# Performance work log

Measured on AMD Instinct MI355X. Metric: run time of the kernel, lower is better.

The kernel has to match this reference:

```python
import jax, jax.numpy as jnp
import numpy as np

B, T, U, D = 2, 512, 48, 512
H, K = 1024, 128  # hidden_channels, num_classes; fc1 in = 2*D = 1024


def setup_inputs() -> dict:
    key = jax.random.key(0)
    ks = jax.random.split(key, 9)
    s = 0.02
    return {
        "img_feature": jax.random.normal(ks[0], (B, T, D), jnp.float32),
        "label_feature": jax.random.normal(ks[1], (B, U, D), jnp.float32),
        "masks": jnp.ones((B, 1, T), jnp.float32),
        "W1": jax.random.normal(ks[2], (H, 2 * D), jnp.float32) * s,
        "b1": jnp.zeros((H,), jnp.float32),
        "W2": jax.random.normal(ks[3], (K, H), jnp.float32) * s,
        "b2": jnp.zeros((K,), jnp.float32),
        "conv_w": jax.random.normal(ks[4], (K, D), jnp.float32) * s,
        "conv_b": jnp.zeros((K,), jnp.float32),
    }


def reference(img_feature, label_feature, masks, W1, b1, W2, b2, conv_w, conv_b):
    # pointwise Conv1d over img features: (B,T,D) -> (B,K,T), masked
    img_seg_score = (jnp.einsum('btd,kd->bkt', img_feature, conv_w)
                     + conv_b[None, :, None]) * masks
    # fc1(cat(label, img)) == label @ Wl^T + img @ Wi^T + b1 (broadcast add),
    # avoiding the O(B*U*T*2D) repeat+cat intermediate.
    d = label_feature.shape[-1]
    Wl, Wi = W1[:, :d], W1[:, d:]
    lab = jnp.einsum('bud,hd->buh', label_feature, Wl)  # (B,U,H)
    img = jnp.einsum('btd,hd->bth', img_feature, Wi)    # (B,T,H)
    h = jnp.tanh(lab[:, :, None, :] + img[:, None, :, :] + b1)  # (B,U,T,H)
    joint = jnp.einsum('buth,kh->butk', h, W2) + b2
    joint_score = jax.nn.log_softmax(joint, axis=-1)
    return (img_seg_score, joint_score)
```

## Files before the change

### kernel.cpp

```cpp
#include <hip/hip_runtime.h>
#include <math.h>

#define BB 2
#define TT 512
#define UU 48
#define DD 512
#define HH 1024
#define KK 128

typedef __bf16 bf16x8 __attribute__((ext_vector_type(8)));
typedef float floatx4 __attribute__((ext_vector_type(4)));

__device__ __forceinline__ float tanh_fast(float x) {
    float x2 = x * x;
    float num = x * fmaf(x2, x2 + 105.0f, 945.0f);
    float den = fmaf(x2, fmaf(x2, 15.0f, 420.0f), 945.0f);
    float r = num * __fdividef(1.0f, den);
    return fminf(1.0f, fmaxf(-1.0f, r));
}

__global__ __launch_bounds__(256) void mid_kernel2(
    const float* __restrict__ img, const float* __restrict__ labf,
    const float* __restrict__ W1, const float* __restrict__ W2,
    const float* __restrict__ conv_w,
    const float* __restrict__ b1, const float* __restrict__ conv_b,
    const float* __restrict__ masks,
    __bf16* __restrict__ imgHb, __bf16* __restrict__ labHb,
    __bf16* __restrict__ W2s, float* __restrict__ seg_out) {
    int bid = blockIdx.x, tid = threadIdx.x;
    if (bid >= 312) {
        int base = (bid - 312) * 256 + tid;
#pragma unroll
        for (int i = 0; i < 32; ++i) {
            int o = base + i * 4096;
            int hg = o >> 10, kk2 = (o >> 3) & 127, hl = o & 7;
            W2s[o] = (__bf16)W2[(size_t)kk2 * HH + hg * 8 + hl];
        }
        return;
    }
    __shared__ __align__(16) __bf16 a_s[32][72];
    __shared__ __align__(16) __bf16 w_s[8192];
    const float* Arow;
    const float* Wbase;
    int r0, n0b, wstride, region;
    if (bid < 256) {
        region = 0; Arow = img; Wbase = W1 + 512; wstride = 1024;
        r0 = (bid & 31) * 32; n0b = (bid >> 5) * 128;
    } else if (bid < 280) {
        region = 1; Arow = labf; Wbase = W1; wstride = 1024;
        int i = bid - 256; r0 = (i % 3) * 32; n0b = (i / 3) * 128;
    } else {
        region = 2; Arow = img; Wbase = conv_w; wstride = 512;
        r0 = (bid - 280) * 32; n0b = 0;
    }
    int lane = tid & 63, wv = tid >> 6;
    int m0 = (wv & 1) * 16, n0w = (wv >> 1) * 64;
    int q = lane >> 4, r = lane & 15;
    int arow = tid >> 3, acol = (tid & 7) * 8;
    floatx4 acc[4] = {};
    for (int c = 0; c < 8; ++c) {
        int cb = c * 64;
        {
            const float* ap = &Arow[(size_t)(r0 + arow) * DD + cb + acol];
            float4 a0 = *(const float4*)ap;
            float4 a1 = *(const float4*)(ap + 4);
            bf16x8 av;
            av[0] = (__bf16)a0.x; av[1] = (__bf16)a0.y;
            av[2] = (__bf16)a0.z; av[3] = (__bf16)a0.w;
            av[4] = (__bf16)a1.x; av[5] = (__bf16)a1.y;
            av[6] = (__bf16)a1.z; av[7] = (__bf16)a1.w;
            *(bf16x8*)&a_s[arow][acol] = av;
        }
#pragma unroll
        for (int i2 = 0; i2 < 4; ++i2) {
            int g = i2 * 256 + tid;
            int kg = g >> 7, n = g & 127;
            const float* wp = &Wbase[(size_t)(n0b + n) * wstride + cb + kg * 8];
            float4 w0 = *(const float4*)wp;
            float4 w1 = *(const float4*)(wp + 4);
            bf16x8 wvv;
            wvv[0] = (__bf16)w0.x; wvv[1] = (__bf16)w0.y;
            wvv[2] = (__bf16)w0.z; wvv[3] = (__bf16)w0.w;
            wvv[4] = (__bf16)w1.x; wvv[5] = (__bf16)w1.y;
            wvv[6] = (__bf16)w1.z; wvv[7] = (__bf16)w1.w;
            *(bf16x8*)&w_s[g * 8] = wvv;
        }
        __syncthreads();
#pragma unroll
        for (int kt = 0; kt < 2; ++kt) {
            bf16x8 af = *(const bf16x8*)&a_s[m0 + r][kt * 32 + q * 8];
#pragma unroll
            for (int nt = 0; nt < 4; ++nt) {
                bf16x8 bfv = *(const bf16x8*)
                    &w_s[((kt * 4 + q) * 128 + n0w + nt * 16 + r) * 8];
                acc[nt] = __builtin_amdgcn_mfma_f32_16x16x32_bf16(
                    af, bfv, acc[nt], 0, 0, 0);
            }
        }
        __syncthreads();
    }
    if (region == 0) {
#pragma unroll
        for (int nt = 0; nt < 4; ++nt) {
            int n = n0b + n0w + nt * 16 + r;
#pragma unroll
            for (int rr = 0; rr < 4; ++rr)
                imgHb[(size_t)(r0 + m0 + 4 * q + rr) * HH + n] =
                    (__bf16)acc[nt][rr];
        }
    } else if (region == 1) {
#pragma unroll
        for (int nt = 0; nt < 4; ++nt) {
            int n = n0b + n0w + nt * 16 + r;
            float bv = b1[n];
#pragma unroll
            for (int rr = 0; rr < 4; ++rr)
                labHb[(size_t)(r0 + m0 + 4 * q + rr) * HH + n] =
                    (__bf16)(acc[nt][rr] + bv);
        }
    } else {
#pragma unroll
        for (int nt = 0; nt < 4; ++nt) {
            int k = n0w + nt * 16 + r;
            float bv = conv_b[k];
#pragma unroll
            for (int rr = 0; rr < 4; ++rr) {
                int row = r0 + m0 + 4 * q + rr;
                int b = row >> 9, t = row & 511;
                seg_out[((size_t)b * KK + k) * TT + t] =
                    (acc[nt][rr] + bv) * masks[row];
            }
        }
    }
}

__global__ __launch_bounds__(256, 3) void joint_kernel3(
    const __bf16* __restrict__ imgHb,
    const __bf16* __restrict__ labHb,
    const __bf16* __restrict__ W2s,
    const float* __restrict__ b2,
    float* __restrict__ out) {
    __shared__ __align__(16) __bf16 h_s[2][64][72];
    __shared__ __align__(16) __bf16 w_s[2][8192];
    int tid = threadIdx.x, bid = blockIdx.x;
    int t0 = (bid & 7) * 64;
    int rest = bid >> 3;
    int u = rest % UU, b = rest / UU;
    const __bf16* imgrow = imgHb + ((size_t)b * TT + t0) * HH;
    const __bf16* labrow = labHb + ((size_t)b * UU + u) * HH;
    int lane = tid & 63, wv = tid >> 6;
    int m0 = wv * 16;
    int q = lane >> 4, r = lane & 15;
    int srow2 = (tid >> 3) * 2, scol = (tid & 7) * 8;
    floatx4 acc[8] = {};
    bf16x8 iv0, iv1, lv, wr0, wr1, wr2, wr3;
    {
        iv0 = *(const bf16x8*)&imgrow[(size_t)srow2 * HH + scol];
        iv1 = *(const bf16x8*)&imgrow[(size_t)(srow2 + 1) * HH + scol];
        lv  = *(const bf16x8*)&labrow[scol];
        wr0 = *(const bf16x8*)&W2s[(0 * 256 + tid) * 8];
        wr1 = *(const bf16x8*)&W2s[(1 * 256 + tid) * 8];
        wr2 = *(const bf16x8*)&W2s[(2 * 256 + tid) * 8];
        wr3 = *(const bf16x8*)&W2s[(3 * 256 + tid) * 8];
    }
#pragma unroll 2
    for (int c = 0; c < 16; ++c) {
        int buf = c & 1;
        *(bf16x8*)&w_s[buf][(0 * 256 + tid) * 8] = wr0;
        *(bf16x8*)&w_s[buf][(1 * 256 + tid) * 8] = wr1;
        *(bf16x8*)&w_s[buf][(2 * 256 + tid) * 8] = wr2;
        *(bf16x8*)&w_s[buf][(3 * 256 + tid) * 8] = wr3;
        {
            bf16x8 h0, h1;
#pragma unroll
            for (int i = 0; i < 8; ++i) {
                float xl = (float)lv[i];
                h0[i] = (__bf16)tanh_fast((float)iv0[i] + xl);
                h1[i] = (__bf16)tanh_fast((float)iv1[i] + xl);
            }
            *(bf16x8*)&h_s[buf][srow2][scol] = h0;
            *(bf16x8*)&h_s[buf][srow2 + 1][scol] = h1;
        }
        __syncthreads();
        if (c < 15) {
            int cb = (c + 1) * 64;
            iv0 = *(const bf16x8*)&imgrow[(size_t)srow2 * HH + cb + scol];
            iv1 = *(const bf16x8*)&imgrow[(size_t)(srow2 + 1) * HH + cb + scol];
            lv  = *(const bf16x8*)&labrow[cb + scol];
            const __bf16* wsrc = W2s + (size_t)cb * KK;
            wr0 = *(const bf16x8*)&wsrc[(0 * 256 + tid) * 8];
            wr1 = *(const bf16x8*)&wsrc[(1 * 256 + tid) * 8];
            wr2 = *(const bf16x8*)&wsrc[(2 * 256 + tid) * 8];
            wr3 = *(const bf16x8*)&wsrc[(3 * 256 + tid) * 8];
        }
#pragma unroll
        for (int kt = 0; kt < 2; ++kt) {
            bf16x8 af = *(const bf16x8*)&h_s[buf][m0 + r][kt * 32 + q * 8];
#pragma unroll
            for (int nt = 0; nt < 8; ++nt) {
                bf16x8 bfv = *(const bf16x8*)
                    &w_s[buf][((kt * 4 + q) * 128 + nt * 16 + r) * 8];
                acc[nt] = __builtin_amdgcn_mfma_f32_16x16x32_bf16(
                    af, bfv, acc[nt], 0, 0, 0);
            }
        }
    }
    float b2v[8];
#pragma unroll
    for (int nt = 0; nt < 8; ++nt) b2v[nt] = b2[nt * 16 + r];
    float* orow = out + (((size_t)b * UU + u) * TT + t0 + m0) * KK;
#pragma unroll
    for (int rr = 0; rr < 4; ++rr) {
        float v[8];
        float mx = -INFINITY;
#pragma unroll
        for (int nt = 0; nt < 8; ++nt) {
            v[nt] = acc[nt][rr] + b2v[nt];
            mx = fmaxf(mx, v[nt]);
        }
        mx = fmaxf(mx, __shfl_xor(mx, 1, 16));
        mx = fmaxf(mx, __shfl_xor(mx, 2, 16));
        mx = fmaxf(mx, __shfl_xor(mx, 4, 16));
        mx = fmaxf(mx, __shfl_xor(mx, 8, 16));
        float s = 0.f;
#pragma unroll
        for (int nt = 0; nt < 8; ++nt) s += __expf(v[nt] - mx);
        s += __shfl_xor(s, 1, 16);
        s += __shfl_xor(s, 2, 16);
        s += __shfl_xor(s, 4, 16);
        s += __shfl_xor(s, 8, 16);
        float lse = mx + __logf(s);
        int row = 4 * q + rr;
#pragma unroll
        for (int nt = 0; nt < 8; ++nt)
            orow[(size_t)row * KK + nt * 16 + r] = v[nt] - lse;
    }
}

extern "C" void kernel_launch(void* const* d_in, const int* in_sizes, int n_in,
                              void* d_out, int out_size, void* d_ws, size_t ws_size,
                              hipStream_t stream) {
    const float* img    = (const float*)d_in[0];
    const float* labf   = (const float*)d_in[1];
    const float* masks  = (const float*)d_in[2];
    const float* W1     = (const float*)d_in[3];
    const float* b1     = (const float*)d_in[4];
    const float* W2     = (const float*)d_in[5];
    const float* b2     = (const float*)d_in[6];
    const float* conv_w = (const float*)d_in[7];
    const float* conv_b = (const float*)d_in[8];
    float* out = (float*)d_out;

    __bf16* base   = (__bf16*)d_ws;
    __bf16* imgHb  = base;
    __bf16* labHb  = imgHb + 1024 * 1024;
    __bf16* W2s    = labHb + 96 * 1024;

    mid_kernel2<<<328, 256, 0, stream>>>(img, labf, W1, W2, conv_w,
                                         b1, conv_b, masks,
                                         imgHb, labHb, W2s, out);
    joint_kernel3<<<768, 256, 0, stream>>>(imgHb, labHb, W2s, b2,
                                           out + (size_t)BB * KK * TT);
}
```

Baseline: 147.9 us.

## Drop LDS staging in joint kernel and prefetch operands in projection kernel

```diff
diff --git a/kernel.cpp b/kernel.cpp
--- a/kernel.cpp
+++ b/kernel.cpp
@@ -19,7 +19,7 @@
     return fminf(1.0f, fmaxf(-1.0f, r));
 }
 
-__global__ __launch_bounds__(256) void mid_kernel2(
+__global__ __launch_bounds__(256) void mid_kernel3(
     const float* __restrict__ img, const float* __restrict__ labf,
     const float* __restrict__ W1, const float* __restrict__ W2,
     const float* __restrict__ conv_w,
@@ -57,35 +57,49 @@
     int m0 = (wv & 1) * 16, n0w = (wv >> 1) * 64;
     int q = lane >> 4, r = lane & 15;
     int arow = tid >> 3, acol = (tid & 7) * 8;
+    int wn = tid >> 3, wk = tid & 7;
+    const float* aptr = &Arow[(size_t)(r0 + arow) * DD + acol];
     floatx4 acc[4] = {};
+    float4 pa0, pa1, pw[4][2];
+    pa0 = *(const float4*)aptr;
+    pa1 = *(const float4*)(aptr + 4);
+#pragma unroll
+    for (int i2 = 0; i2 < 4; ++i2) {
+        const float* wp_ = &Wbase[(size_t)(n0b + i2 * 32 + wn) * wstride + wk * 8];
+        pw[i2][0] = *(const float4*)wp_;
+        pw[i2][1] = *(const float4*)(wp_ + 4);
+    }
     for (int c = 0; c < 8; ++c) {
-        int cb = c * 64;
         {
-            const float* ap = &Arow[(size_t)(r0 + arow) * DD + cb + acol];
-            float4 a0 = *(const float4*)ap;
-            float4 a1 = *(const float4*)(ap + 4);
             bf16x8 av;
-            av[0] = (__bf16)a0.x; av[1] = (__bf16)a0.y;
-            av[2] = (__bf16)a0.z; av[3] = (__bf16)a0.w;
-            av[4] = (__bf16)a1.x; av[5] = (__bf16)a1.y;
-            av[6] = (__bf16)a1.z; av[7] = (__bf16)a1.w;
+            av[0] = (__bf16)pa0.x; av[1] = (__bf16)pa0.y;
+            av[2] = (__bf16)pa0.z; av[3] = (__bf16)pa0.w;
+            av[4] = (__bf16)pa1.x; av[5] = (__bf16)pa1.y;
+            av[6] = (__bf16)pa1.z; av[7] = (__bf16)pa1.w;
             *(bf16x8*)&a_s[arow][acol] = av;
-        }
-#pragma unroll
-        for (int i2 = 0; i2 < 4; ++i2) {
-            int g = i2 * 256 + tid;
-            int kg = g >> 7, n = g & 127;
-            const float* wp = &Wbase[(size_t)(n0b + n) * wstride + cb + kg * 8];
-            float4 w0 = *(const float4*)wp;
-            float4 w1 = *(const float4*)(wp + 4);
-            bf16x8 wvv;
-            wvv[0] = (__bf16)w0.x; wvv[1] = (__bf16)w0.y;
-            wvv[2] = (__bf16)w0.z; wvv[3] = (__bf16)w0.w;
-            wvv[4] = (__bf16)w1.x; wvv[5] = (__bf16)w1.y;
-            wvv[6] = (__bf16)w1.z; wvv[7] = (__bf16)w1.w;
-            *(bf16x8*)&w_s[g * 8] = wvv;
+#pragma unroll
+            for (int i2 = 0; i2 < 4; ++i2) {
+                bf16x8 wvv;
+                wvv[0] = (__bf16)pw[i2][0].x; wvv[1] = (__bf16)pw[i2][0].y;
+                wvv[2] = (__bf16)pw[i2][0].z; wvv[3] = (__bf16)pw[i2][0].w;
+                wvv[4] = (__bf16)pw[i2][1].x; wvv[5] = (__bf16)pw[i2][1].y;
+                wvv[6] = (__bf16)pw[i2][1].z; wvv[7] = (__bf16)pw[i2][1].w;
+                *(bf16x8*)&w_s[((size_t)wk * 128 + i2 * 32 + wn) * 8] = wvv;
+            }
         }
         __syncthreads();
+        if (c < 7) {
+            int cb = (c + 1) * 64;
+            pa0 = *(const float4*)(aptr + cb);
+            pa1 = *(const float4*)(aptr + cb + 4);
+#pragma unroll
+            for (int i2 = 0; i2 < 4; ++i2) {
+                const float* wp_ =
+                    &Wbase[(size_t)(n0b + i2 * 32 + wn) * wstride + cb + wk * 8];
+                pw[i2][0] = *(const float4*)wp_;
+                pw[i2][1] = *(const float4*)(wp_ + 4);
+            }
+        }
 #pragma unroll
         for (int kt = 0; kt < 2; ++kt) {
             bf16x8 af = *(const bf16x8*)&a_s[m0 + r][kt * 32 + q * 8];
@@ -134,81 +148,59 @@
     }
 }
 
-__global__ __launch_bounds__(256, 3) void joint_kernel3(
+__global__ __launch_bounds__(256) void joint_kernel4(
     const __bf16* __restrict__ imgHb,
     const __bf16* __restrict__ labHb,
     const __bf16* __restrict__ W2s,
     const float* __restrict__ b2,
     float* __restrict__ out) {
-    __shared__ __align__(16) __bf16 h_s[2][64][72];
-    __shared__ __align__(16) __bf16 w_s[2][8192];
     int tid = threadIdx.x, bid = blockIdx.x;
     int t0 = (bid & 7) * 64;
     int rest = bid >> 3;
     int u = rest % UU, b = rest / UU;
-    const __bf16* imgrow = imgHb + ((size_t)b * TT + t0) * HH;
-    const __bf16* labrow = labHb + ((size_t)b * UU + u) * HH;
     int lane = tid & 63, wv = tid >> 6;
-    int m0 = wv * 16;
     int q = lane >> 4, r = lane & 15;
-    int srow2 = (tid >> 3) * 2, scol = (tid & 7) * 8;
+    const __bf16* imgrow = imgHb + ((size_t)b * TT + t0 + wv * 16 + r) * HH;
+    const __bf16* labrow = labHb + (size_t)(b * UU + u) * HH;
+    const __bf16* wbase = W2s + q * 1024 + r * 8;
+    int c0 = q * 8, c1 = 32 + q * 8;
     floatx4 acc[8] = {};
-    bf16x8 iv0, iv1, lv, wr0, wr1, wr2, wr3;
-    {
-        iv0 = *(const bf16x8*)&imgrow[(size_t)srow2 * HH + scol];
-        iv1 = *(const bf16x8*)&imgrow[(size_t)(srow2 + 1) * HH + scol];
-        lv  = *(const bf16x8*)&labrow[scol];
-        wr0 = *(const bf16x8*)&W2s[(0 * 256 + tid) * 8];
-        wr1 = *(const bf16x8*)&W2s[(1 * 256 + tid) * 8];
-        wr2 = *(const bf16x8*)&W2s[(2 * 256 + tid) * 8];
-        wr3 = *(const bf16x8*)&W2s[(3 * 256 + tid) * 8];
-    }
-#pragma unroll 2
+    bf16x8 ivA = *(const bf16x8*)&imgrow[c0];
+    bf16x8 ivB = *(const bf16x8*)&imgrow[c1];
+    bf16x8 lvA = *(const bf16x8*)&labrow[c0];
+    bf16x8 lvB = *(const bf16x8*)&labrow[c1];
     for (int c = 0; c < 16; ++c) {
-        int buf = c & 1;
-        *(bf16x8*)&w_s[buf][(0 * 256 + tid) * 8] = wr0;
-        *(bf16x8*)&w_s[buf][(1 * 256 + tid) * 8] = wr1;
-        *(bf16x8*)&w_s[buf][(2 * 256 + tid) * 8] = wr2;
-        *(bf16x8*)&w_s[buf][(3 * 256 + tid) * 8] = wr3;
-        {
-            bf16x8 h0, h1;
-#pragma unroll
-            for (int i = 0; i < 8; ++i) {
-                float xl = (float)lv[i];
-                h0[i] = (__bf16)tanh_fast((float)iv0[i] + xl);
-                h1[i] = (__bf16)tanh_fast((float)iv1[i] + xl);
-            }
-            *(bf16x8*)&h_s[buf][srow2][scol] = h0;
-            *(bf16x8*)&h_s[buf][srow2 + 1][scol] = h1;
-        }
-        __syncthreads();
+        bf16x8 a0, a1;
+#pragma unroll
+        for (int i = 0; i < 8; ++i) {
+            a0[i] = (__bf16)tanh_fast((float)ivA[i] + (float)lvA[i]);
+            a1[i] = (__bf16)tanh_fast((float)ivB[i] + (float)lvB[i]);
+        }
         if (c < 15) {
             int cb = (c + 1) * 64;
-            iv0 = *(const bf16x8*)&imgrow[(size_t)srow2 * HH + cb + scol];
-            iv1 = *(const bf16x8*)&imgrow[(size_t)(srow2 + 1) * HH + cb + scol];
-            lv  = *(const bf16x8*)&labrow[cb + scol];
-            const __bf16* wsrc = W2s + (size_t)cb * KK;
-            wr0 = *(const bf16x8*)&wsrc[(0 * 256 + tid) * 8];
-            wr1 = *(const bf16x8*)&wsrc[(1 * 256 + tid) * 8];
-            wr2 = *(const bf16x8*)&wsrc[(2 * 256 + tid) * 8];
-            wr3 = *(const bf16x8*)&wsrc[(3 * 256 + tid) * 8];
-        }
-#pragma unroll
-        for (int kt = 0; kt < 2; ++kt) {
-            bf16x8 af = *(const bf16x8*)&h_s[buf][m0 + r][kt * 32 + q * 8];
-#pragma unroll
-            for (int nt = 0; nt < 8; ++nt) {
-                bf16x8 bfv = *(const bf16x8*)
-                    &w_s[buf][((kt * 4 + q) * 128 + nt * 16 + r) * 8];
-                acc[nt] = __builtin_amdgcn_mfma_f32_16x16x32_bf16(
-                    af, bfv, acc[nt], 0, 0, 0);
-            }
+            ivA = *(const bf16x8*)&imgrow[cb + c0];
+            ivB = *(const bf16x8*)&imgrow[cb + c1];
+            lvA = *(const bf16x8*)&labrow[cb + c0];
+            lvB = *(const bf16x8*)&labrow[cb + c1];
+        }
+        const __bf16* wc = wbase + (size_t)c * 8192;
+#pragma unroll
+        for (int nt = 0; nt < 8; ++nt) {
+            bf16x8 bf0 = *(const bf16x8*)&wc[nt * 128];
+            acc[nt] = __builtin_amdgcn_mfma_f32_16x16x32_bf16(
+                a0, bf0, acc[nt], 0, 0, 0);
+        }
+#pragma unroll
+        for (int nt = 0; nt < 8; ++nt) {
+            bf16x8 bf1 = *(const bf16x8*)&wc[4096 + nt * 128];
+            acc[nt] = __builtin_amdgcn_mfma_f32_16x16x32_bf16(
+                a1, bf1, acc[nt], 0, 0, 0);
         }
     }
     float b2v[8];
 #pragma unroll
     for (int nt = 0; nt < 8; ++nt) b2v[nt] = b2[nt * 16 + r];
-    float* orow = out + (((size_t)b * UU + u) * TT + t0 + m0) * KK;
+    float* orow = out + (((size_t)b * UU + u) * TT + t0 + wv * 16) * KK;
 #pragma unroll
     for (int rr = 0; rr < 4; ++rr) {
         float v[8];
@@ -256,9 +248,9 @@
     __bf16* labHb  = imgHb + 1024 * 1024;
     __bf16* W2s    = labHb + 96 * 1024;
 
-    mid_kernel2<<<328, 256, 0, stream>>>(img, labf, W1, W2, conv_w,
+    mid_kernel3<<<328, 256, 0, stream>>>(img, labf, W1, W2, conv_w,
                                          b1, conv_b, masks,
                                          imgHb, labHb, W2s, out);
-    joint_kernel3<<<768, 256, 0, stream>>>(imgHb, labHb, W2s, b2,
+    joint_kernel4<<<768, 256, 0, stream>>>(imgHb, labHb, W2s, b2,
                                            out + (size_t)BB * KK * TT);
 }
```

Result: slower. 172.7 us (+16.7%).
